# Performance work log

Hardware: AMD Instinct MI355X
Metric: run time of the kernel (lower is better)

The kernel has to match this reference:

```python
import jax, jax.numpy as jnp
import numpy as np

N_NODES = 50000
N_EDGES = 800000
D = 128
N_LAYERS = 4
N_GRAPHS = 512
N_CLASS = 10


def setup_inputs() -> dict:
    key = jax.random.key(0)
    ks = jax.random.split(key, 12)
    x = jax.random.normal(ks[0], (N_NODES, D), dtype=jnp.float32)
    edge_index = jax.random.randint(ks[1], (2, N_EDGES), 0, N_NODES, dtype=jnp.int64)
    batch = jnp.sort(jax.random.randint(ks[2], (N_NODES,), 0, N_GRAPHS, dtype=jnp.int64))
    s = 1.0 / np.sqrt(D)
    W_conv = jax.random.uniform(ks[3], (N_LAYERS, D, D), jnp.float32, -s, s)
    b_conv = jnp.zeros((N_LAYERS, D), jnp.float32)
    W1 = jax.random.uniform(ks[4], (D, D), jnp.float32, -s, s)
    b1 = jnp.zeros((D,), jnp.float32)
    W2 = jax.random.uniform(ks[5], (D, D // 2), jnp.float32, -s, s)
    b2 = jnp.zeros((D // 2,), jnp.float32)
    W3 = jax.random.uniform(ks[6], (D // 2, N_CLASS), jnp.float32, -1.0 / np.sqrt(D // 2), 1.0 / np.sqrt(D // 2))
    b3 = jnp.zeros((N_CLASS,), jnp.float32)
    return {"x": x, "edge_index": edge_index, "batch": batch,
            "W_conv": W_conv, "b_conv": b_conv,
            "W1": W1, "b1": b1, "W2": W2, "b2": b2, "W3": W3, "b3": b3}


def reference(x, edge_index, batch, W_conv, b_conv, W1, b1, W2, b2, W3, b3):
    row, col = edge_index[0], edge_index[1]  # messages: source=row -> target=col
    # GCN symmetric normalization with self-loops (PyG GCNConv default).
    deg = jax.ops.segment_sum(jnp.ones((row.shape[0],), x.dtype), col, num_segments=N_NODES) + 1.0
    dinv = jax.lax.rsqrt(deg)
    edge_norm = (dinv[row] * dinv[col])[:, None]      # [E,1]
    self_norm = (1.0 / deg)[:, None]                  # [N,1] = dinv_i * dinv_i

    def gcn_layer(h, W, b):
        h = h @ W                                      # [N,D]
        agg = jax.ops.segment_sum(h[row] * edge_norm, col, num_segments=N_NODES)
        agg = agg + h * self_norm                      # self-loop contribution
        return jax.nn.relu(agg + b)

    h = x
    for l in range(N_LAYERS):
        h = gcn_layer(h, W_conv[l], b_conv[l])

    # global_add_pool over graph ids
    g = jax.ops.segment_sum(h, batch, num_segments=N_GRAPHS)  # [G,D]

    # MLP head (dropout is identity in eval mode)
    g = jax.nn.relu(g @ W1 + b1)
    g = jax.nn.relu(g @ W2 + b2)
    return g @ W3 + b3
```

## Files before the change

kernel.cpp:

```cpp
#include <hip/hip_runtime.h>
#include <stdint.h>
#include <stddef.h>

#define NN 50000
#define NE 800000
#define DD 128
#define NL 4
#define NG 512
#define NC 10
#define NB 196
#define BCAP 5056
#define GPB 49

using short8 = __attribute__((ext_vector_type(8))) short;
using f32x4  = __attribute__((ext_vector_type(4))) float;

__device__ __forceinline__ float bf2f(unsigned short u) {
  union { unsigned int i; float f; } c; c.i = ((unsigned int)u) << 16; return c.f;
}
__device__ __forceinline__ unsigned short f2bf(float f) {
  union { unsigned int i; float f; } c; c.f = f;
  unsigned int i = c.i;
  return (unsigned short)((i + 0x7FFFu + ((i >> 16) & 1u)) >> 16);
}
__device__ __forceinline__ unsigned int pack2(float a, float b) {
  return (unsigned int)f2bf(a) | ((unsigned int)f2bf(b) << 16);
}
__device__ __forceinline__ void acc8(float* a, uint4 p) {
  a[0] += bf2f((unsigned short)(p.x & 0xffffu)); a[1] += bf2f((unsigned short)(p.x >> 16));
  a[2] += bf2f((unsigned short)(p.y & 0xffffu)); a[3] += bf2f((unsigned short)(p.y >> 16));
  a[4] += bf2f((unsigned short)(p.z & 0xffffu)); a[5] += bf2f((unsigned short)(p.z >> 16));
  a[6] += bf2f((unsigned short)(p.w & 0xffffu)); a[7] += bf2f((unsigned short)(p.w >> 16));
}

__global__ __launch_bounds__(1024) void p1b_k(const int* __restrict__ erow,
                                              const int* __restrict__ ecol,
                                              int* __restrict__ cursor,
                                              unsigned int* __restrict__ ebuf) {
  __shared__ int lcnt[NB], gb[NB];
  int tid = threadIdx.x;
  if (tid < NB) lcnt[tid] = 0;
  __syncthreads();
  int e0 = blockIdx.x * 4096 + tid;
  int bk[4], sl[4]; unsigned int pk[4];
#pragma unroll
  for (int j = 0; j < 4; ++j) {
    int e = e0 + j * 1024;
    bk[j] = -1;
    if (e < NE) {
      int d = ecol[e], s = erow[e];
      bk[j] = d >> 8;
      pk[j] = ((unsigned int)(d & 255) << 16) | (unsigned int)s;
      sl[j] = atomicAdd(&lcnt[bk[j]], 1);
    }
  }
  __syncthreads();
  if (tid < NB) {
    int c = lcnt[tid];
    gb[tid] = c ? atomicAdd(&cursor[tid], c) : 0;
  }
  __syncthreads();
#pragma unroll
  for (int j = 0; j < 4; ++j)
    if (bk[j] >= 0) ebuf[(size_t)bk[j] * BCAP + gb[bk[j]] + sl[j]] = pk[j];
}

__global__ __launch_bounds__(1024) void p2_k(const unsigned int* __restrict__ ebuf,
                                             const int* __restrict__ cursor,
                                             const float* __restrict__ x,
                                             const int* __restrict__ batch,
                                             const float* __restrict__ Wc,
                                             int* __restrict__ csr_ptr,
                                             int* __restrict__ csr_end,
                                             int* __restrict__ csr_src,
                                             float* __restrict__ dinv,
                                             unsigned short* __restrict__ xb,
                                             int* __restrict__ gptr,
                                             unsigned short* __restrict__ Wbt) {
  int b = blockIdx.x, tid = threadIdx.x;
  if (b >= NB + GPB) {
    int l = b - NB - GPB;
    const float* W = Wc + (size_t)l * DD * DD;
    unsigned short* WT = Wbt + (size_t)l * DD * DD;
    for (int i = tid; i < DD * DD; i += 1024) {
      int n = i >> 7, k = i & 127;
      WT[n * DD + k] = f2bf(W[k * DD + n]);
    }
    return;
  }
  if (b >= NB) {
    int i = (b - NB) * 1024 + tid;
    if (i >= NN) return;
    int bb = batch[i];
    int bp = (i == 0) ? -1 : batch[i - 1];
    for (int g = bp + 1; g <= bb; ++g) gptr[g] = i;
    if (i == NN - 1) { for (int g = bb + 1; g <= NG; ++g) gptr[g] = NN; }
    return;
  }

  __shared__ unsigned int pr[BCAP];
  __shared__ int srcb[BCAP];
  __shared__ int hist_s[256], scn[256], lcur[256];
  __shared__ float dinv_s[256];
  size_t beg = (size_t)b * BCAP;
  int cnt = cursor[b];
  if (cnt > BCAP) cnt = BCAP;

  if (tid < 256) hist_s[tid] = 0;
  __syncthreads();
  for (int i = tid; i < cnt; i += 1024) {
    unsigned int p = ebuf[beg + i];
    pr[i] = p;
    atomicAdd(&hist_s[p >> 16], 1);
  }
  __syncthreads();
  if (tid < 256) scn[tid] = hist_s[tid];
  __syncthreads();
  for (int off = 1; off < 256; off <<= 1) {
    int v = (tid < 256 && tid >= off) ? scn[tid - off] : 0;
    __syncthreads();
    if (tid < 256) scn[tid] += v;
    __syncthreads();
  }
  if (tid < 256) {
    int ex = scn[tid] - hist_s[tid];
    lcur[tid] = ex;
    int V = b * 256 + tid;
    if (V < NN) {
      csr_ptr[V] = (int)beg + ex;
      csr_end[V] = (int)beg + scn[tid];
      float dv = rsqrtf((float)(hist_s[tid] + 1));
      dinv[V] = dv;
      dinv_s[tid] = dv;
    }
  }
  __syncthreads();
  for (int i = tid; i < cnt; i += 1024) {
    unsigned int p = pr[i];
    int pos = atomicAdd(&lcur[p >> 16], 1);
    srcb[pos] = (int)(p & 0xFFFFu);
  }
  __syncthreads();
  for (int i = tid; i < cnt; i += 1024) csr_src[beg + i] = srcb[i];

  for (int i4 = tid; i4 < 256 * 32; i4 += 1024) {
    int vl = i4 >> 5;
    int V = b * 256 + vl;
    if (V < NN) {
      float d = dinv_s[vl];
      int q = i4 & 31;
      f32x4 vx = *((const f32x4*)(x + (size_t)V * DD) + q);
      uint2 o;
      o.x = pack2(vx[0] * d, vx[1] * d);
      o.y = pack2(vx[2] * d, vx[3] * d);
      ((uint2*)(xb + (size_t)V * DD))[q] = o;
    }
  }
}

__global__ __launch_bounds__(256) void agg_k(const unsigned short* __restrict__ hs,
                                             unsigned short* __restrict__ agg,
                                             const int* __restrict__ csr_ptr,
                                             const int* __restrict__ csr_end,
                                             const int* __restrict__ csr_src,
                                             const float* __restrict__ dinv) {
  int v = blockIdx.x * 4 + (threadIdx.x >> 6);
  if (v >= NN) return;
  int lane = threadIdx.x & 63;
  int qg = lane >> 4, r = lane & 15;
  const uint4* rows = (const uint4*)hs;

  float a[8] = {0.f, 0.f, 0.f, 0.f, 0.f, 0.f, 0.f, 0.f};
  float b[8] = {0.f, 0.f, 0.f, 0.f, 0.f, 0.f, 0.f, 0.f};
  if (qg == 0) acc8(a, rows[(size_t)v * 16 + r]);

  int e = csr_ptr[v] + qg, end = csr_end[v];
  for (; e + 12 < end; e += 16) {
    int s0 = csr_src[e];
    int s1 = csr_src[e + 4];
    int s2 = csr_src[e + 8];
    int s3 = csr_src[e + 12];
    uint4 p0 = rows[(size_t)s0 * 16 + r];
    uint4 p1 = rows[(size_t)s1 * 16 + r];
    uint4 p2 = rows[(size_t)s2 * 16 + r];
    uint4 p3 = rows[(size_t)s3 * 16 + r];
    acc8(a, p0); acc8(b, p1); acc8(a, p2); acc8(b, p3);
  }
  for (; e + 4 < end; e += 8) {
    int s0 = csr_src[e];
    int s1 = csr_src[e + 4];
    uint4 p0 = rows[(size_t)s0 * 16 + r];
    uint4 p1 = rows[(size_t)s1 * 16 + r];
    acc8(a, p0); acc8(b, p1);
  }
  if (e < end) acc8(a, rows[(size_t)csr_src[e] * 16 + r]);

#pragma unroll
  for (int t = 0; t < 8; ++t) a[t] += b[t];
#pragma unroll
  for (int t = 0; t < 8; ++t) {
    a[t] += __shfl_xor(a[t], 16, 64);
    a[t] += __shfl_xor(a[t], 32, 64);
  }

  if (qg == 0) {
    float dv = dinv[v];
    uint4 o;
    o.x = pack2(dv * a[0], dv * a[1]);
    o.y = pack2(dv * a[2], dv * a[3]);
    o.z = pack2(dv * a[4], dv * a[5]);
    o.w = pack2(dv * a[6], dv * a[7]);
    *((uint4*)(agg + (size_t)v * DD) + r) = o;
  }
}

__global__ __launch_bounds__(256) void gemm_relu_k(const unsigned short* __restrict__ A,
                                                   const unsigned short* __restrict__ Wb,
                                                   const float* __restrict__ bias,
                                                   unsigned short* __restrict__ out,
                                                   const float* __restrict__ dscale,
                                                   int M) {
  __shared__ unsigned short Wt[128][136];
  int tid = threadIdx.x;
  for (int i = tid; i < 128 * 16; i += 256) {
    int rr = i >> 4, c = i & 15;
    *(uint4*)&Wt[rr][c * 8] = *(const uint4*)(Wb + rr * DD + c * 8);
  }
  __syncthreads();

  int wave = tid >> 6, lane = tid & 63;
  int q = lane >> 4, r = lane & 15;
  int row0 = blockIdx.x * 64 + wave * 16;

  int arow = row0 + r;
  if (arow > M - 1) arow = M - 1;
  const short* Arow = (const short*)A + (size_t)arow * DD;

  short8 afrag[4];
#pragma unroll
  for (int ks = 0; ks < 4; ++ks)
    afrag[ks] = *(const short8*)(Arow + ks * 32 + q * 8);

  f32x4 acc[8];
#pragma unroll
  for (int ct = 0; ct < 8; ++ct) acc[ct] = (f32x4){0.f, 0.f, 0.f, 0.f};

#pragma unroll
  for (int ks = 0; ks < 4; ++ks) {
#pragma unroll
    for (int ct = 0; ct < 8; ++ct) {
      short8 bfrag = *(const short8*)(&Wt[ct * 16 + r][ks * 32 + q * 8]);
      acc[ct] = __builtin_amdgcn_mfma_f32_16x16x32_bf16(afrag[ks], bfrag, acc[ct], 0, 0, 0);
    }
  }

  int orow = row0 + q * 4;
  float sc[4];
#pragma unroll
  for (int reg = 0; reg < 4; ++reg) {
    int rr = orow + reg;
    sc[reg] = (dscale && rr < M) ? dscale[rr] : 1.f;
  }
#pragma unroll
  for (int ct = 0; ct < 8; ++ct) {
    int coln = ct * 16 + r;
    float bc = bias[coln];
#pragma unroll
    for (int reg = 0; reg < 4; ++reg) {
      int rr = orow + reg;
      if (rr < M) {
        float val = fmaxf(acc[ct][reg] + bc, 0.f) * sc[reg];
        out[(size_t)rr * DD + coln] = f2bf(val);
      }
    }
  }
}

__global__ __launch_bounds__(128) void poolmlp_k(const unsigned short* __restrict__ h,
                                                 const int* __restrict__ gptr,
                                                 const float* __restrict__ W1,
                                                 const float* __restrict__ b1,
                                                 const float* __restrict__ W2,
                                                 const float* __restrict__ b2,
                                                 const float* __restrict__ W3,
                                                 const float* __restrict__ b3,
                                                 float* __restrict__ out) {
  __shared__ float s_g[128], s_h1[128], s_h2[64];
  int g = blockIdx.x, t = threadIdx.x;
  int beg = gptr[g], end = gptr[g + 1];
  float acc = 0.f;
  for (int v = beg; v < end; ++v) acc += bf2f(h[(size_t)v * DD + t]);
  s_g[t] = acc;
  __syncthreads();
  {
    float a = b1[t];
    for (int k = 0; k < 128; ++k) a += s_g[k] * W1[k * 128 + t];
    s_h1[t] = fmaxf(a, 0.f);
  }
  __syncthreads();
  if (t < 64) {
    float a = b2[t];
    for (int k = 0; k < 128; ++k) a += s_h1[k] * W2[k * 64 + t];
    s_h2[t] = fmaxf(a, 0.f);
  }
  __syncthreads();
  if (t < NC) {
    float a = b3[t];
    for (int k = 0; k < 64; ++k) a += s_h2[k] * W3[k * NC + t];
    out[g * NC + t] = a;
  }
}


extern "C" void kernel_launch(void* const* d_in, const int* in_sizes, int n_in,
                              void* d_out, int out_size, void* d_ws, size_t ws_size,
                              hipStream_t stream) {
  const float* x     = (const float*)d_in[0];
  const int*   ei    = (const int*)d_in[1];
  const int*   batch = (const int*)d_in[2];
  const float* Wc    = (const float*)d_in[3];
  const float* bc    = (const float*)d_in[4];
  const float* W1    = (const float*)d_in[5];
  const float* b1    = (const float*)d_in[6];
  const float* W2    = (const float*)d_in[7];
  const float* b2    = (const float*)d_in[8];
  const float* W3    = (const float*)d_in[9];
  const float* b3    = (const float*)d_in[10];
  float* out = (float*)d_out;

  const int* erow = ei;
  const int* ecol = ei + NE;

  char* w = (char*)d_ws;
  int*   cursor  = (int*)w;    w += NB * 4;
  int*   csr_ptr = (int*)w;    w += (size_t)(NN + 4) * 4;
  int*   csr_end = (int*)w;    w += (size_t)(NN + 4) * 4;
  int*   gptr    = (int*)w;    w += (NG + 4) * 4;
  int*   csr_src = (int*)w;    w += (size_t)NB * BCAP * 4;
  float* dinv    = (float*)w;  w += (size_t)NN * 4;
  w = (char*)(((uintptr_t)w + 255) & ~(uintptr_t)255);
  unsigned short* Wbt  = (unsigned short*)w; w += (size_t)NL * DD * DD * 2;
  unsigned short* xb   = (unsigned short*)w; w += (size_t)NN * DD * 2;
  unsigned short* aggb = (unsigned short*)w; w += (size_t)NN * DD * 2;
  unsigned short* hA   = (unsigned short*)w; w += (size_t)NN * DD * 2;
  unsigned short* hB   = (unsigned short*)w; w += (size_t)NN * DD * 2;
  unsigned int* ebuf = (unsigned int*)hA;

  hipMemsetAsync(cursor, 0, NB * 4, stream);

  p1b_k<<<NB, 1024, 0, stream>>>(erow, ecol, cursor, ebuf);
  p2_k <<<NB + GPB + NL, 1024, 0, stream>>>(ebuf, cursor, x, batch, Wc, csr_ptr,
                                            csr_end, csr_src, dinv, xb, gptr, Wbt);

  const int aggGrid  = (NN + 3) / 4;
  const int gemmGrid = (NN + 63) / 64;

  for (int l = 0; l < NL; ++l) {
    const unsigned short* hin = (l == 0) ? xb : ((l & 1) ? hA : hB);
    unsigned short* dst = (l & 1) ? hB : hA;
    const float* dsc = (l == NL - 1) ? nullptr : dinv;
    agg_k<<<aggGrid, 256, 0, stream>>>(hin, aggb, csr_ptr, csr_end, csr_src, dinv);
    gemm_relu_k<<<gemmGrid, 256, 0, stream>>>(aggb, Wbt + (size_t)l * DD * DD,
                                              bc + (size_t)l * DD, dst, dsc, NN);
  }

  poolmlp_k<<<NG, 128, 0, stream>>>(hB, gptr, W1, b1, W2, b2, W3, b3, out);

  (void)in_sizes; (void)n_in; (void)out_size; (void)ws_size;
}
```

Baseline: 329.4 us.

## Fuse neighbor aggregation and GEMM into one per-layer kernel via LDS tile

Merges the sparse aggregation kernel and the MFMA GEMM+ReLU kernel into a single 512-thread kernel per layer. Each block aggregates 64 node rows into a shared-memory tile (8 nodes per wave), then the 8 waves split the 64x128 GEMM into row and column halves. This removes the round trip of the aggregated buffer through global memory and halves the kernel launches. In exchange, each wave serializes its 8 node gathers, there is less parallelism for the irregular gather, and LDS use grows, which may lower occupancy.

New measurement: 391.7 us. +18.9%, slower.

```diff
diff --git a/kernel.cpp b/kernel.cpp
--- a/kernel.cpp
+++ b/kernel.cpp
@@ -158,117 +158,118 @@
   }
 }
 
-__global__ __launch_bounds__(256) void agg_k(const unsigned short* __restrict__ hs,
-                                             unsigned short* __restrict__ agg,
-                                             const int* __restrict__ csr_ptr,
-                                             const int* __restrict__ csr_end,
-                                             const int* __restrict__ csr_src,
-                                             const float* __restrict__ dinv) {
-  int v = blockIdx.x * 4 + (threadIdx.x >> 6);
-  if (v >= NN) return;
-  int lane = threadIdx.x & 63;
-  int qg = lane >> 4, r = lane & 15;
-  const uint4* rows = (const uint4*)hs;
-
-  float a[8] = {0.f, 0.f, 0.f, 0.f, 0.f, 0.f, 0.f, 0.f};
-  float b[8] = {0.f, 0.f, 0.f, 0.f, 0.f, 0.f, 0.f, 0.f};
-  if (qg == 0) acc8(a, rows[(size_t)v * 16 + r]);
-
-  int e = csr_ptr[v] + qg, end = csr_end[v];
-  for (; e + 12 < end; e += 16) {
-    int s0 = csr_src[e];
-    int s1 = csr_src[e + 4];
-    int s2 = csr_src[e + 8];
-    int s3 = csr_src[e + 12];
-    uint4 p0 = rows[(size_t)s0 * 16 + r];
-    uint4 p1 = rows[(size_t)s1 * 16 + r];
-    uint4 p2 = rows[(size_t)s2 * 16 + r];
-    uint4 p3 = rows[(size_t)s3 * 16 + r];
-    acc8(a, p0); acc8(b, p1); acc8(a, p2); acc8(b, p3);
-  }
-  for (; e + 4 < end; e += 8) {
-    int s0 = csr_src[e];
-    int s1 = csr_src[e + 4];
-    uint4 p0 = rows[(size_t)s0 * 16 + r];
-    uint4 p1 = rows[(size_t)s1 * 16 + r];
-    acc8(a, p0); acc8(b, p1);
-  }
-  if (e < end) acc8(a, rows[(size_t)csr_src[e] * 16 + r]);
-
-#pragma unroll
-  for (int t = 0; t < 8; ++t) a[t] += b[t];
-#pragma unroll
-  for (int t = 0; t < 8; ++t) {
-    a[t] += __shfl_xor(a[t], 16, 64);
-    a[t] += __shfl_xor(a[t], 32, 64);
-  }
-
-  if (qg == 0) {
-    float dv = dinv[v];
-    uint4 o;
-    o.x = pack2(dv * a[0], dv * a[1]);
-    o.y = pack2(dv * a[2], dv * a[3]);
-    o.z = pack2(dv * a[4], dv * a[5]);
-    o.w = pack2(dv * a[6], dv * a[7]);
-    *((uint4*)(agg + (size_t)v * DD) + r) = o;
-  }
-}
-
-__global__ __launch_bounds__(256) void gemm_relu_k(const unsigned short* __restrict__ A,
-                                                   const unsigned short* __restrict__ Wb,
-                                                   const float* __restrict__ bias,
-                                                   unsigned short* __restrict__ out,
-                                                   const float* __restrict__ dscale,
-                                                   int M) {
+__global__ __launch_bounds__(512, 4) void fused_layer_k(
+    const unsigned short* __restrict__ hs,
+    const unsigned short* __restrict__ Wb,
+    const float* __restrict__ bias,
+    unsigned short* __restrict__ out,
+    const float* __restrict__ dscale,
+    const int* __restrict__ csr_ptr,
+    const int* __restrict__ csr_end,
+    const int* __restrict__ csr_src,
+    const float* __restrict__ dinv) {
   __shared__ unsigned short Wt[128][136];
+  __shared__ unsigned short At[64][136];
+
   int tid = threadIdx.x;
-  for (int i = tid; i < 128 * 16; i += 256) {
+  for (int i = tid; i < 128 * 16; i += 512) {
     int rr = i >> 4, c = i & 15;
     *(uint4*)&Wt[rr][c * 8] = *(const uint4*)(Wb + rr * DD + c * 8);
   }
-  __syncthreads();
 
   int wave = tid >> 6, lane = tid & 63;
-  int q = lane >> 4, r = lane & 15;
-  int row0 = blockIdx.x * 64 + wave * 16;
-
-  int arow = row0 + r;
-  if (arow > M - 1) arow = M - 1;
-  const short* Arow = (const short*)A + (size_t)arow * DD;
+  int qg = lane >> 4, r = lane & 15;
+  int row0 = blockIdx.x * 64;
+  const uint4* rows = (const uint4*)hs;
+
+  for (int i = 0; i < 8; ++i) {
+    int av = wave * 8 + i;
+    int v = row0 + av;
+    if (v < NN) {
+      float a[8] = {0.f, 0.f, 0.f, 0.f, 0.f, 0.f, 0.f, 0.f};
+      float b[8] = {0.f, 0.f, 0.f, 0.f, 0.f, 0.f, 0.f, 0.f};
+      if (qg == 0) acc8(a, rows[(size_t)v * 16 + r]);
+      int e = csr_ptr[v] + qg, end = csr_end[v];
+      for (; e + 12 < end; e += 16) {
+        int s0 = csr_src[e];
+        int s1 = csr_src[e + 4];
+        int s2 = csr_src[e + 8];
+        int s3 = csr_src[e + 12];
+        uint4 p0 = rows[(size_t)s0 * 16 + r];
+        uint4 p1 = rows[(size_t)s1 * 16 + r];
+        uint4 p2 = rows[(size_t)s2 * 16 + r];
+        uint4 p3 = rows[(size_t)s3 * 16 + r];
+        acc8(a, p0); acc8(b, p1); acc8(a, p2); acc8(b, p3);
+      }
+      for (; e + 4 < end; e += 8) {
+        int s0 = csr_src[e];
+        int s1 = csr_src[e + 4];
+        uint4 p0 = rows[(size_t)s0 * 16 + r];
+        uint4 p1 = rows[(size_t)s1 * 16 + r];
+        acc8(a, p0); acc8(b, p1);
+      }
+      if (e < end) acc8(a, rows[(size_t)csr_src[e] * 16 + r]);
+
+#pragma unroll
+      for (int t = 0; t < 8; ++t) a[t] += b[t];
+#pragma unroll
+      for (int t = 0; t < 8; ++t) {
+        a[t] += __shfl_xor(a[t], 16, 64);
+        a[t] += __shfl_xor(a[t], 32, 64);
+      }
+      if (qg == 0) {
+        float dv = dinv[v];
+        uint4 o;
+        o.x = pack2(dv * a[0], dv * a[1]);
+        o.y = pack2(dv * a[2], dv * a[3]);
+        o.z = pack2(dv * a[4], dv * a[5]);
+        o.w = pack2(dv * a[6], dv * a[7]);
+        *(uint4*)&At[av][r * 8] = o;
+      }
+    } else if (qg == 0) {
+      uint4 z; z.x = 0u; z.y = 0u; z.z = 0u; z.w = 0u;
+      *(uint4*)&At[av][r * 8] = z;
+    }
+  }
+  __syncthreads();
+
+  int rh = wave >> 1, ch = wave & 1;
+  int q = qg;
+  int arowL = rh * 16 + r;
 
   short8 afrag[4];
 #pragma unroll
   for (int ks = 0; ks < 4; ++ks)
-    afrag[ks] = *(const short8*)(Arow + ks * 32 + q * 8);
-
-  f32x4 acc[8];
-#pragma unroll
-  for (int ct = 0; ct < 8; ++ct) acc[ct] = (f32x4){0.f, 0.f, 0.f, 0.f};
+    afrag[ks] = *(const short8*)&At[arowL][ks * 32 + q * 8];
+
+  f32x4 acc[4];
+#pragma unroll
+  for (int ct = 0; ct < 4; ++ct) acc[ct] = (f32x4){0.f, 0.f, 0.f, 0.f};
 
 #pragma unroll
   for (int ks = 0; ks < 4; ++ks) {
 #pragma unroll
-    for (int ct = 0; ct < 8; ++ct) {
-      short8 bfrag = *(const short8*)(&Wt[ct * 16 + r][ks * 32 + q * 8]);
+    for (int ct = 0; ct < 4; ++ct) {
+      short8 bfrag = *(const short8*)(&Wt[ch * 64 + ct * 16 + r][ks * 32 + q * 8]);
       acc[ct] = __builtin_amdgcn_mfma_f32_16x16x32_bf16(afrag[ks], bfrag, acc[ct], 0, 0, 0);
     }
   }
 
-  int orow = row0 + q * 4;
+  int orow = row0 + rh * 16 + q * 4;
   float sc[4];
 #pragma unroll
   for (int reg = 0; reg < 4; ++reg) {
     int rr = orow + reg;
-    sc[reg] = (dscale && rr < M) ? dscale[rr] : 1.f;
-  }
-#pragma unroll
-  for (int ct = 0; ct < 8; ++ct) {
-    int coln = ct * 16 + r;
+    sc[reg] = (dscale && rr < NN) ? dscale[rr] : 1.f;
+  }
+#pragma unroll
+  for (int ct = 0; ct < 4; ++ct) {
+    int coln = ch * 64 + ct * 16 + r;
     float bc = bias[coln];
 #pragma unroll
     for (int reg = 0; reg < 4; ++reg) {
       int rr = orow + reg;
-      if (rr < M) {
+      if (rr < NN) {
         float val = fmaxf(acc[ct][reg] + bc, 0.f) * sc[reg];
         out[(size_t)rr * DD + coln] = f2bf(val);
       }
@@ -352,19 +353,19 @@
   p2_k <<<NB + GPB + NL, 1024, 0, stream>>>(ebuf, cursor, x, batch, Wc, csr_ptr,
                                             csr_end, csr_src, dinv, xb, gptr, Wbt);
 
-  const int aggGrid  = (NN + 3) / 4;
-  const int gemmGrid = (NN + 63) / 64;
+  const int fusedGrid = (NN + 63) / 64;
 
   for (int l = 0; l < NL; ++l) {
     const unsigned short* hin = (l == 0) ? xb : ((l & 1) ? hA : hB);
     unsigned short* dst = (l & 1) ? hB : hA;
     const float* dsc = (l == NL - 1) ? nullptr : dinv;
-    agg_k<<<aggGrid, 256, 0, stream>>>(hin, aggb, csr_ptr, csr_end, csr_src, dinv);
-    gemm_relu_k<<<gemmGrid, 256, 0, stream>>>(aggb, Wbt + (size_t)l * DD * DD,
-                                              bc + (size_t)l * DD, dst, dsc, NN);
+    fused_layer_k<<<fusedGrid, 512, 0, stream>>>(hin, Wbt + (size_t)l * DD * DD,
+                                                 bc + (size_t)l * DD, dst, dsc,
+                                                 csr_ptr, csr_end, csr_src, dinv);
   }
 
   poolmlp_k<<<NG, 128, 0, stream>>>(hB, gptr, W1, b1, W2, b2, W3, b3, out);
 
   (void)in_sizes; (void)n_in; (void)out_size; (void)ws_size;
-}
+  (void)aggb;
+}
```
